# Kernel tuning notes

Measured on AMD Instinct MI355X. Metric: run time of the kernel, lower is better.

The kernel has to match this reference:

```python
import jax, jax.numpy as jnp
import numpy as np

B, S, E, H = 4, 2048, 1024, 16
D = E // H  # head_dim = 64


def setup_inputs() -> dict:
    key = jax.random.key(0)
    ks = jax.random.split(key, 9)
    s = 1.0 / np.sqrt(E)
    return {
        "x": jax.random.normal(ks[0], (B, S, E), dtype=jnp.float32),
        "mask": jnp.ones((B, S), dtype=jnp.int32),
        "Wq": jax.random.uniform(ks[1], (E, E), jnp.float32, -s, s),
        "bq": jnp.zeros((E,), jnp.float32),
        "Wk": jax.random.uniform(ks[2], (E, E), jnp.float32, -s, s),
        "bk": jnp.zeros((E,), jnp.float32),
        "Wv": jax.random.uniform(ks[3], (E, E), jnp.float32, -s, s),
        "bv": jnp.zeros((E,), jnp.float32),
        "Wo": jax.random.uniform(ks[4], (E, E), jnp.float32, -s, s),
        "bo": jnp.zeros((E,), jnp.float32),
    }


def reference(x, mask, Wq, bq, Wk, bk, Wv, bv, Wo, bo):
    # projections: weights stored as (in, out)
    q = x @ Wq + bq  # [B,S,E]
    k = x @ Wk + bk
    v = x @ Wv + bv
    # split heads: b s (h d) -> b h s d
    q = q.reshape(B, S, H, D).transpose(0, 2, 1, 3)
    k = k.reshape(B, S, H, D).transpose(0, 2, 1, 3)
    v = v.reshape(B, S, H, D).transpose(0, 2, 1, 3)
    scale = 1.0 / np.sqrt(D).astype(np.float32)
    dot = jnp.einsum('bhsd,bhtd->bhst', q, k) * scale  # [B,H,S,S]
    # key padding mask: 1 = valid, 0 = masked
    neg_inf = jnp.asarray(-jnp.inf, dot.dtype)
    dot = jnp.where(mask[:, None, None, :] == 0, neg_inf, dot)
    attn = jax.nn.softmax(dot, axis=-1)
    o = jnp.einsum('bhst,bhtd->bhsd', attn, v)  # [B,H,S,D]
    o = o.transpose(0, 2, 1, 3).reshape(B, S, E)  # merge heads
    return o @ Wo + bo
```

## Files before the change

### kernel.cpp

```cpp
#include <hip/hip_runtime.h>

#define Bc 4
#define Sc 2048
#define Ec 1024
#define Hc 16
#define Dc 64
#define BSc 8192
#define KVB 64

typedef short bf16x8 __attribute__((ext_vector_type(8)));
typedef float f32x4 __attribute__((ext_vector_type(4)));
typedef unsigned short u16;
typedef unsigned long long u64;

__device__ __forceinline__ u16 f2bf(float f){
  unsigned u = __builtin_bit_cast(unsigned, f);
  u += 0x7FFFu + ((u >> 16) & 1u);
  return (u16)(u >> 16);
}
__device__ __forceinline__ void gll16(const void* g, void* l){
  __builtin_amdgcn_global_load_lds((const __attribute__((address_space(1))) void*)g,
                                   (__attribute__((address_space(3))) void*)l, 16, 0, 0);
}
__device__ __forceinline__ float exp2_s(float x){
#if __has_builtin(__builtin_amdgcn_exp2f)
  return __builtin_amdgcn_exp2f(x);
#else
  float r;
  asm volatile("v_exp_f32 %0, %1\n\ts_nop 1" : "=v"(r) : "v"(x));
  return r;
#endif
}
__device__ __forceinline__ unsigned cvtpk(float a, float b){
  unsigned r;
  asm volatile("v_cvt_pk_bf16_f32 %0, %1, %2\n\ts_nop 1" : "=v"(r) : "v"(a), "v"(b));
  return r;
}

__global__ void cvt_x_kernel(const float* __restrict__ x, u16* __restrict__ xb, int n){
  int i = (blockIdx.x * 256 + threadIdx.x) * 4;
  if (i >= n) return;
  float4 v = *(const float4*)(x + i);
  *(ushort4*)(xb+i) = make_ushort4(f2bf(v.x), f2bf(v.y), f2bf(v.z), f2bf(v.w));
}

__global__ void wt_kernel(const float* __restrict__ w0, const float* __restrict__ w1,
                          const float* __restrict__ w2, const float* __restrict__ w3,
                          u16* __restrict__ wt){
  const float* w = blockIdx.z==0 ? w0 : blockIdx.z==1 ? w1 : blockIdx.z==2 ? w2 : w3;
  u16* ho = wt + (size_t)blockIdx.z * Ec * Ec;
  __shared__ float t[32][33];
  int k0 = blockIdx.y * 32, n0 = blockIdx.x * 32;
  int tx = threadIdx.x & 31, ty = threadIdx.x >> 5;
  for (int i = 0; i < 4; ++i){
    int k = ty + i*8;
    t[k][tx] = w[(size_t)(k0+k)*Ec + n0 + tx];
  }
  __syncthreads();
  for (int i = 0; i < 4; ++i){
    int nn = ty + i*8;
    ho[(size_t)(n0+nn)*Ec + k0 + tx] = f2bf(t[tx][nn]);
  }
}

__global__ __launch_bounds__(256, 2)
void gemm_qkv(const u16* __restrict__ A, const u16* __restrict__ Wt,
              const float* __restrict__ bq, const float* __restrict__ bk,
              const float* __restrict__ bv,
              u16* __restrict__ qout, u16* __restrict__ kout, u16* __restrict__ vout)
{
  constexpr int K = Ec;
  __shared__ alignas(16) u16 As[128*32];
  __shared__ alignas(16) u16 Bs[128*32];
  const int tid = threadIdx.x, lane = tid & 63, w = tid >> 6;
  const int wr = w >> 1, wc = w & 1;
  const int m0 = blockIdx.y * 128;
  const int n0g = blockIdx.x * 128;
  const int which = n0g >> 10;
  const int n0 = n0g & 1023;
  const u16* Bt = Wt + (size_t)which * Ec * Ec;
  const float* bias = which == 0 ? bq : which == 1 ? bk : bv;
  const int l15 = lane & 15, kslot = lane >> 4;
  const f32x4 fz = {0.f,0.f,0.f,0.f};
  f32x4 acc[4][4];
  for (int i=0;i<4;++i) for (int j=0;j<4;++j) acc[i][j] = fz;

  const int srow = lane >> 2, sslot = lane & 3;

  for (int k0 = 0; k0 < K; k0 += 32){
    __syncthreads();
    for (int i = 0; i < 2; ++i){
      int c = w*2 + i;
      int row = c*16 + srow;
      int sw = (row ^ (row >> 2)) & 3;
      gll16(A  + (size_t)(m0+row)*K + k0 + ((sslot ^ sw) << 3), As + c*512);
      gll16(Bt + (size_t)(n0+row)*K + k0 + ((sslot ^ sw) << 3), Bs + c*512);
    }
    __syncthreads();
    bf16x8 af[4], bfr[4];
    for (int mi = 0; mi < 4; ++mi){
      int row = wr*64 + mi*16 + l15;
      int sw = (row ^ (row >> 2)) & 3;
      af[mi] = *(const bf16x8*)(As + row*32 + ((kslot ^ sw) << 3));
    }
    for (int ni = 0; ni < 4; ++ni){
      int row = wc*64 + ni*16 + l15;
      int sw = (row ^ (row >> 2)) & 3;
      bfr[ni] = *(const bf16x8*)(Bs + row*32 + ((kslot ^ sw) << 3));
    }
    for (int mi = 0; mi < 4; ++mi)
      for (int ni = 0; ni < 4; ++ni)
        acc[mi][ni] = __builtin_amdgcn_mfma_f32_16x16x32_bf16(af[mi], bfr[ni], acc[mi][ni], 0, 0, 0);
  }

  for (int mi = 0; mi < 4; ++mi){
    for (int ni = 0; ni < 4; ++ni){
      int col = n0 + wc*64 + ni*16 + l15;
      int row0 = m0 + wr*64 + mi*16 + kslot*4;
      float bi = bias[col];
      if (which == 2){
        int bb = row0 >> 11, s0 = row0 & 2047;
        int hh = col >> 6, dd = col & 63;
        ushort4 pk = make_ushort4(f2bf(acc[mi][ni][0]+bi), f2bf(acc[mi][ni][1]+bi),
                                  f2bf(acc[mi][ni][2]+bi), f2bf(acc[mi][ni][3]+bi));
        *(ushort4*)(vout + ((size_t)(bb*Hc+hh)*Dc + dd)*Sc + s0) = pk;
      } else {
        u16* dst = which == 0 ? qout : kout;
        for (int j = 0; j < 4; ++j){
          float v = acc[mi][ni][j] + bi;
          int row = row0 + j;
          float vv = (which == 0) ? v * 0.18033688f : v;
          int bb = row >> 11, ss = row & 2047;
          int hh = col >> 6, dd = col & 63;
          dst[((size_t)(bb*Hc+hh)*Sc + ss)*Dc + dd] = f2bf(vv);
        }
      }
    }
  }
}

__global__ __launch_bounds__(256, 2)
void gemm_out(const u16* __restrict__ A, const u16* __restrict__ Bt,
              const float* __restrict__ bias, float* __restrict__ outp)
{
  constexpr int K = Ec;
  __shared__ alignas(16) u16 As[128*32];
  __shared__ alignas(16) u16 Bs[128*32];
  const int tid = threadIdx.x, lane = tid & 63, w = tid >> 6;
  const int wr = w >> 1, wc = w & 1;
  const int m0 = blockIdx.y * 128, n0 = blockIdx.x * 128;
  const int l15 = lane & 15, kslot = lane >> 4;
  const f32x4 fz = {0.f,0.f,0.f,0.f};
  f32x4 acc[4][4];
  for (int i=0;i<4;++i) for (int j=0;j<4;++j) acc[i][j] = fz;

  const int srow = lane >> 2, sslot = lane & 3;

  for (int k0 = 0; k0 < K; k0 += 32){
    __syncthreads();
    for (int i = 0; i < 2; ++i){
      int c = w*2 + i;
      int row = c*16 + srow;
      int sw = (row ^ (row >> 2)) & 3;
      gll16(A  + (size_t)(m0+row)*K + k0 + ((sslot ^ sw) << 3), As + c*512);
      gll16(Bt + (size_t)(n0+row)*K + k0 + ((sslot ^ sw) << 3), Bs + c*512);
    }
    __syncthreads();
    bf16x8 af[4], bfr[4];
    for (int mi = 0; mi < 4; ++mi){
      int row = wr*64 + mi*16 + l15;
      int sw = (row ^ (row >> 2)) & 3;
      af[mi] = *(const bf16x8*)(As + row*32 + ((kslot ^ sw) << 3));
    }
    for (int ni = 0; ni < 4; ++ni){
      int row = wc*64 + ni*16 + l15;
      int sw = (row ^ (row >> 2)) & 3;
      bfr[ni] = *(const bf16x8*)(Bs + row*32 + ((kslot ^ sw) << 3));
    }
    for (int mi = 0; mi < 4; ++mi)
      for (int ni = 0; ni < 4; ++ni)
        acc[mi][ni] = __builtin_amdgcn_mfma_f32_16x16x32_bf16(af[mi], bfr[ni], acc[mi][ni], 0, 0, 0);
  }

  for (int mi = 0; mi < 4; ++mi){
    for (int ni = 0; ni < 4; ++ni){
      int col = n0 + wc*64 + ni*16 + l15;
      int row0 = m0 + wr*64 + mi*16 + kslot*4;
      float bi = bias[col];
      for (int j = 0; j < 4; ++j)
        outp[(size_t)(row0+j)*Ec + col] = acc[mi][ni][j] + bi;
    }
  }
}

__global__ __launch_bounds__(256, 2)
void attn_kernel(const u16* __restrict__ qb, const u16* __restrict__ kb,
                 const u16* __restrict__ vt, const int* __restrict__ mask,
                 u16* __restrict__ ob)
{
  __shared__ alignas(16) u16 Ks[2][KVB*Dc];
  __shared__ alignas(16) u16 Vs[2][Dc*KVB];
  const int tid = threadIdx.x, lane = tid & 63, w = tid >> 6;
  const int l15 = lane & 15, ks = lane >> 4;
  const int wg = ((blockIdx.x & 7) << 7) | (blockIdx.x >> 3);
  const int bh = wg >> 4, qblk = wg & 15;
  const int b = bh >> 4, h = bh & 15;
  const int q0 = qblk*128 + w*32;

  const u16* Q  = qb + (size_t)bh*Sc*Dc;
  const u16* Kg = kb + (size_t)bh*Sc*Dc;
  const u16* Vg = vt + (size_t)bh*Dc*Sc;
  const int* mpb = mask + b*Sc;

  int nzl = 1;
  {
    const int4* mv4 = (const int4*)mpb;
#pragma unroll
    for (int i = 0; i < 8; ++i){
      int4 v = mv4[i*64 + lane];
      nzl &= (v.x && v.y && v.z && v.w) ? 1 : 0;
    }
  }
  const bool allvalid = __all(nzl);

  int koff[2], voff[2];
#pragma unroll
  for (int i = 0; i < 2; ++i){
    int S = (w*2+i)*64 + lane;
    int row = S >> 3, s = S & 7;
    koff[i] = row*Dc + ((s ^ (row & 7)) << 3);
    voff[i] = row*Sc + ((s ^ (row & 7)) << 3);
  }
  const int Xl = (l15 & 7) << 4;

  bf16x8 qf[2][2];
#pragma unroll
  for (int qa = 0; qa < 2; ++qa)
#pragma unroll
    for (int kd = 0; kd < 2; ++kd)
      qf[qa][kd] = *(const bf16x8*)(Q + (size_t)(q0 + qa*16 + l15)*Dc + kd*32 + ks*8);

  bf16x8 onesb;
#pragma unroll
  for (int j = 0; j < 8; ++j) onesb[j] = (short)0x3F80;

  const f32x4 fz = {0.f,0.f,0.f,0.f};
  f32x4 o[2][4];
#pragma unroll
  for (int qa = 0; qa < 2; ++qa)
#pragma unroll
    for (int db = 0; db < 4; ++db) o[qa][db] = fz;
  float m[2] = {-3e38f, -3e38f}, runl[2] = {0.f, 0.f};

#pragma unroll
  for (int i = 0; i < 2; ++i){
    gll16(Kg + koff[i], &Ks[0][(w*2+i)*512]);
    gll16(Vg + voff[i], &Vs[0][(w*2+i)*512]);
  }

  const int NT = Sc / KVB;
  int cur = 0;
  for (int t = 0; t < NT; ++t){
    asm volatile("s_waitcnt vmcnt(0)" ::: "memory");
    __syncthreads();
    if (t + 1 < NT){
      const u16* kg = Kg + (size_t)(t+1)*(KVB*Dc);
      const u16* vg = Vg + (size_t)(t+1)*KVB;
#pragma unroll
      for (int i = 0; i < 2; ++i){
        gll16(kg + koff[i], &Ks[cur^1][(w*2+i)*512]);
        gll16(vg + voff[i], &Vs[cur^1][(w*2+i)*512]);
      }
    }
    const char* Ksb = (const char*)&Ks[cur][0];
    const char* Vsb = (const char*)&Vs[cur][0];

    f32x4 sc[4][2];
#pragma unroll
    for (int nb = 0; nb < 4; ++nb){
      bf16x8 kf0 = *(const bf16x8*)(Ksb + nb*2048 + l15*128 + (((0*4+ks) << 4) ^ Xl));
      bf16x8 kf1 = *(const bf16x8*)(Ksb + nb*2048 + l15*128 + (((1*4+ks) << 4) ^ Xl));
#pragma unroll
      for (int qa = 0; qa < 2; ++qa){
        sc[nb][qa] = __builtin_amdgcn_mfma_f32_16x16x32_bf16(kf0, qf[qa][0], fz, 0,0,0);
        sc[nb][qa] = __builtin_amdgcn_mfma_f32_16x16x32_bf16(kf1, qf[qa][1], sc[nb][qa], 0,0,0);
      }
    }
    if (!allvalid){
      const int* mp = mpb + t*KVB;
#pragma unroll
      for (int nb = 0; nb < 4; ++nb)
#pragma unroll
        for (int r = 0; r < 4; ++r){
          float bi = mp[nb*16 + ks*4 + r] ? 0.f : -3e38f;
          sc[nb][0][r] += bi;
          sc[nb][1][r] += bi;
        }
    }
    float pmax[2];
#pragma unroll
    for (int qa = 0; qa < 2; ++qa){
      f32x4 mx4;
#pragma unroll
      for (int r = 0; r < 4; ++r)
        mx4[r] = fmaxf(fmaxf(sc[0][qa][r], sc[1][qa][r]),
                       fmaxf(sc[2][qa][r], sc[3][qa][r]));
      pmax[qa] = fmaxf(fmaxf(mx4[0], mx4[1]), fmaxf(mx4[2], mx4[3]));
    }
    int ok = (t > 0) && (pmax[0] <= m[0] + 8.f) && (pmax[1] <= m[1] + 8.f);
    if (!__all(ok)){
#pragma unroll
      for (int qa = 0; qa < 2; ++qa){
        float tv = pmax[qa];
        tv = fmaxf(tv, __shfl_xor(tv, 16, 64));
        tv = fmaxf(tv, __shfl_xor(tv, 32, 64));
        float nm = fmaxf(m[qa], tv);
        float al = exp2_s(m[qa] - nm);
        m[qa] = nm;
        runl[qa] *= al;
#pragma unroll
        for (int db = 0; db < 4; ++db)
#pragma unroll
          for (int r = 0; r < 4; ++r)
            o[qa][db][r] *= al;
      }
    }
#pragma unroll
    for (int nb = 0; nb < 4; ++nb)
#pragma unroll
      for (int qa = 0; qa < 2; ++qa)
#pragma unroll
        for (int r = 0; r < 4; ++r)
          sc[nb][qa][r] = exp2_s(sc[nb][qa][r] - m[qa]);

    f32x4 accl[2] = {fz, fz};
#pragma unroll
    for (int kt = 0; kt < 2; ++kt){
      bf16x8 pb[2];
#pragma unroll
      for (int qa = 0; qa < 2; ++qa){
        union { bf16x8 v; unsigned u[4]; } pu;
        pu.u[0] = cvtpk(sc[2*kt  ][qa][0], sc[2*kt  ][qa][1]);
        pu.u[1] = cvtpk(sc[2*kt  ][qa][2], sc[2*kt  ][qa][3]);
        pu.u[2] = cvtpk(sc[2*kt+1][qa][0], sc[2*kt+1][qa][1]);
        pu.u[3] = cvtpk(sc[2*kt+1][qa][2], sc[2*kt+1][qa][3]);
        pb[qa] = pu.v;
      }
      accl[0] = __builtin_amdgcn_mfma_f32_16x16x32_bf16(onesb, pb[0], accl[0], 0,0,0);
      accl[1] = __builtin_amdgcn_mfma_f32_16x16x32_bf16(onesb, pb[1], accl[1], 0,0,0);
#pragma unroll
      for (int db = 0; db < 4; ++db){
        union { bf16x8 v; u64 q[2]; } vu;
        const int g0 = kt*4 + (ks >> 1);
        const int base = db*2048 + l15*128 + (ks & 1)*8;
        vu.q[0] = *(const u64*)(Vsb + base + (((g0    ) << 4) ^ Xl));
        vu.q[1] = *(const u64*)(Vsb + base + (((g0 + 2) << 4) ^ Xl));
#pragma unroll
        for (int qa = 0; qa < 2; ++qa)
          o[qa][db] = __builtin_amdgcn_mfma_f32_16x16x32_bf16(vu.v, pb[qa], o[qa][db], 0,0,0);
      }
    }
    runl[0] += accl[0][0];
    runl[1] += accl[1][0];
    cur ^= 1;
  }
#pragma unroll
  for (int qa = 0; qa < 2; ++qa){
    float inv = __builtin_amdgcn_rcpf(fmaxf(runl[qa], 1e-35f));
    u16* orow = ob + ((size_t)(b*Sc + q0 + qa*16 + l15))*Ec + h*Dc + ks*4;
#pragma unroll
    for (int db = 0; db < 4; ++db){
      ushort4 pk = make_ushort4(f2bf(o[qa][db][0]*inv), f2bf(o[qa][db][1]*inv),
                                f2bf(o[qa][db][2]*inv), f2bf(o[qa][db][3]*inv));
      *(ushort4*)(orow + db*16) = pk;
    }
  }
}

extern "C" void kernel_launch(void* const* d_in, const int* in_sizes, int n_in,
                              void* d_out, int out_size, void* d_ws, size_t ws_size,
                              hipStream_t stream) {
  const float* x  = (const float*)d_in[0];
  const int* mask = (const int*)d_in[1];
  const float* Wq = (const float*)d_in[2];
  const float* bq = (const float*)d_in[3];
  const float* Wk = (const float*)d_in[4];
  const float* bk = (const float*)d_in[5];
  const float* Wv = (const float*)d_in[6];
  const float* bv = (const float*)d_in[7];
  const float* Wo = (const float*)d_in[8];
  const float* bo = (const float*)d_in[9];
  float* out = (float*)d_out;

  u16* ws   = (u16*)d_ws;
  u16* x_bf = ws;
  u16* w_t  = x_bf + (size_t)BSc*Ec;
  u16* q_bf = w_t  + (size_t)4*Ec*Ec;
  u16* k_bf = q_bf + (size_t)BSc*Ec;
  u16* v_t  = k_bf + (size_t)BSc*Ec;
  u16* o_bf = v_t  + (size_t)BSc*Ec;

  cvt_x_kernel<<<BSc*Ec/1024, 256, 0, stream>>>(x, x_bf, BSc*Ec);
  wt_kernel<<<dim3(32,32,4), 256, 0, stream>>>(Wq, Wk, Wv, Wo, w_t);

  const size_t WSZ = (size_t)Ec*Ec;
  gemm_qkv<<<dim3(24,64), 256, 0, stream>>>(x_bf, w_t, bq, bk, bv, q_bf, k_bf, v_t);

  attn_kernel<<<dim3(1024), 256, 0, stream>>>(q_bf, k_bf, v_t, mask, o_bf);

  gemm_out<<<dim3(8,64), 256, 0, stream>>>(o_bf, w_t+3*WSZ, bo, out);
}
```

Measured before the change: 204.3 us.

## Double per-wave query rows in attention to reuse K/V tiles across 64 queries

Each attention wave now handles 64 query rows (four 16-row groups) instead of 32, so a workgroup covers 256 queries and the grid halves to 512 blocks. Every K/V tile loaded into LDS and every fragment read from it feeds twice as many MFMAs, which cuts global and LDS traffic per unit of work. It also swaps the inline-asm v_cvt_pk_bf16 and v_exp fallback for a software bf16 rounding and plain exp2f, which costs more VALU work. The risks are higher register pressure under launch_bounds(256,2) with possible spills, and fewer blocks to spread across the CUs.

```diff
diff --git a/kernel.cpp b/kernel.cpp
--- a/kernel.cpp
+++ b/kernel.cpp
@@ -26,15 +26,8 @@
 #if __has_builtin(__builtin_amdgcn_exp2f)
   return __builtin_amdgcn_exp2f(x);
 #else
-  float r;
-  asm volatile("v_exp_f32 %0, %1\n\ts_nop 1" : "=v"(r) : "v"(x));
-  return r;
+  return exp2f(x);
 #endif
-}
-__device__ __forceinline__ unsigned cvtpk(float a, float b){
-  unsigned r;
-  asm volatile("v_cvt_pk_bf16_f32 %0, %1, %2\n\ts_nop 1" : "=v"(r) : "v"(a), "v"(b));
-  return r;
 }
 
 __global__ void cvt_x_kernel(const float* __restrict__ x, u16* __restrict__ xb, int n){
@@ -202,10 +195,10 @@
   __shared__ alignas(16) u16 Vs[2][Dc*KVB];
   const int tid = threadIdx.x, lane = tid & 63, w = tid >> 6;
   const int l15 = lane & 15, ks = lane >> 4;
-  const int wg = ((blockIdx.x & 7) << 7) | (blockIdx.x >> 3);
-  const int bh = wg >> 4, qblk = wg & 15;
+  const int wg = ((blockIdx.x & 7) << 6) | (blockIdx.x >> 3);
+  const int bh = wg >> 3, qblk = wg & 7;
   const int b = bh >> 4, h = bh & 15;
-  const int q0 = qblk*128 + w*32;
+  const int q0 = qblk*256 + w*64;
 
   const u16* Q  = qb + (size_t)bh*Sc*Dc;
   const u16* Kg = kb + (size_t)bh*Sc*Dc;
@@ -233,9 +226,9 @@
   }
   const int Xl = (l15 & 7) << 4;
 
-  bf16x8 qf[2][2];
-#pragma unroll
-  for (int qa = 0; qa < 2; ++qa)
+  bf16x8 qf[4][2];
+#pragma unroll
+  for (int qa = 0; qa < 4; ++qa)
 #pragma unroll
     for (int kd = 0; kd < 2; ++kd)
       qf[qa][kd] = *(const bf16x8*)(Q + (size_t)(q0 + qa*16 + l15)*Dc + kd*32 + ks*8);
@@ -245,12 +238,12 @@
   for (int j = 0; j < 8; ++j) onesb[j] = (short)0x3F80;
 
   const f32x4 fz = {0.f,0.f,0.f,0.f};
-  f32x4 o[2][4];
-#pragma unroll
-  for (int qa = 0; qa < 2; ++qa)
+  f32x4 o[4][4];
+#pragma unroll
+  for (int qa = 0; qa < 4; ++qa)
 #pragma unroll
     for (int db = 0; db < 4; ++db) o[qa][db] = fz;
-  float m[2] = {-3e38f, -3e38f}, runl[2] = {0.f, 0.f};
+  float m[4] = {-3e38f,-3e38f,-3e38f,-3e38f}, runl[4] = {0.f,0.f,0.f,0.f};
 
 #pragma unroll
   for (int i = 0; i < 2; ++i){
@@ -275,13 +268,13 @@
     const char* Ksb = (const char*)&Ks[cur][0];
     const char* Vsb = (const char*)&Vs[cur][0];
 
-    f32x4 sc[4][2];
+    f32x4 sc[4][4];
 #pragma unroll
     for (int nb = 0; nb < 4; ++nb){
       bf16x8 kf0 = *(const bf16x8*)(Ksb + nb*2048 + l15*128 + (((0*4+ks) << 4) ^ Xl));
       bf16x8 kf1 = *(const bf16x8*)(Ksb + nb*2048 + l15*128 + (((1*4+ks) << 4) ^ Xl));
 #pragma unroll
-      for (int qa = 0; qa < 2; ++qa){
+      for (int qa = 0; qa < 4; ++qa){
         sc[nb][qa] = __builtin_amdgcn_mfma_f32_16x16x32_bf16(kf0, qf[qa][0], fz, 0,0,0);
         sc[nb][qa] = __builtin_amdgcn_mfma_f32_16x16x32_bf16(kf1, qf[qa][1], sc[nb][qa], 0,0,0);
       }
@@ -293,13 +286,13 @@
 #pragma unroll
         for (int r = 0; r < 4; ++r){
           float bi = mp[nb*16 + ks*4 + r] ? 0.f : -3e38f;
-          sc[nb][0][r] += bi;
-          sc[nb][1][r] += bi;
+#pragma unroll
+          for (int qa = 0; qa < 4; ++qa) sc[nb][qa][r] += bi;
         }
     }
-    float pmax[2];
-#pragma unroll
-    for (int qa = 0; qa < 2; ++qa){
+    float pmax[4];
+#pragma unroll
+    for (int qa = 0; qa < 4; ++qa){
       f32x4 mx4;
 #pragma unroll
       for (int r = 0; r < 4; ++r)
@@ -307,10 +300,11 @@
                        fmaxf(sc[2][qa][r], sc[3][qa][r]));
       pmax[qa] = fmaxf(fmaxf(mx4[0], mx4[1]), fmaxf(mx4[2], mx4[3]));
     }
-    int ok = (t > 0) && (pmax[0] <= m[0] + 8.f) && (pmax[1] <= m[1] + 8.f);
+    int ok = (t > 0) && (pmax[0] <= m[0] + 8.f) && (pmax[1] <= m[1] + 8.f)
+                     && (pmax[2] <= m[2] + 8.f) && (pmax[3] <= m[3] + 8.f);
     if (!__all(ok)){
 #pragma unroll
-      for (int qa = 0; qa < 2; ++qa){
+      for (int qa = 0; qa < 4; ++qa){
         float tv = pmax[qa];
         tv = fmaxf(tv, __shfl_xor(tv, 16, 64));
         tv = fmaxf(tv, __shfl_xor(tv, 32, 64));
@@ -328,26 +322,26 @@
 #pragma unroll
     for (int nb = 0; nb < 4; ++nb)
 #pragma unroll
-      for (int qa = 0; qa < 2; ++qa)
+      for (int qa = 0; qa < 4; ++qa)
 #pragma unroll
         for (int r = 0; r < 4; ++r)
           sc[nb][qa][r] = exp2_s(sc[nb][qa][r] - m[qa]);
 
-    f32x4 accl[2] = {fz, fz};
+    f32x4 accl[4] = {fz, fz, fz, fz};
 #pragma unroll
     for (int kt = 0; kt < 2; ++kt){
-      bf16x8 pb[2];
-#pragma unroll
-      for (int qa = 0; qa < 2; ++qa){
-        union { bf16x8 v; unsigned u[4]; } pu;
-        pu.u[0] = cvtpk(sc[2*kt  ][qa][0], sc[2*kt  ][qa][1]);
-        pu.u[1] = cvtpk(sc[2*kt  ][qa][2], sc[2*kt  ][qa][3]);
-        pu.u[2] = cvtpk(sc[2*kt+1][qa][0], sc[2*kt+1][qa][1]);
-        pu.u[3] = cvtpk(sc[2*kt+1][qa][2], sc[2*kt+1][qa][3]);
-        pb[qa] = pu.v;
-      }
-      accl[0] = __builtin_amdgcn_mfma_f32_16x16x32_bf16(onesb, pb[0], accl[0], 0,0,0);
-      accl[1] = __builtin_amdgcn_mfma_f32_16x16x32_bf16(onesb, pb[1], accl[1], 0,0,0);
+      bf16x8 pb[4];
+#pragma unroll
+      for (int qa = 0; qa < 4; ++qa){
+        bf16x8 tb;
+#pragma unroll
+        for (int r = 0; r < 4; ++r){
+          tb[r]     = (short)f2bf(sc[2*kt  ][qa][r]);
+          tb[4 + r] = (short)f2bf(sc[2*kt+1][qa][r]);
+        }
+        pb[qa] = tb;
+        accl[qa] = __builtin_amdgcn_mfma_f32_16x16x32_bf16(onesb, pb[qa], accl[qa], 0,0,0);
+      }
 #pragma unroll
       for (int db = 0; db < 4; ++db){
         union { bf16x8 v; u64 q[2]; } vu;
@@ -356,16 +350,16 @@
         vu.q[0] = *(const u64*)(Vsb + base + (((g0    ) << 4) ^ Xl));
         vu.q[1] = *(const u64*)(Vsb + base + (((g0 + 2) << 4) ^ Xl));
 #pragma unroll
-        for (int qa = 0; qa < 2; ++qa)
+        for (int qa = 0; qa < 4; ++qa)
           o[qa][db] = __builtin_amdgcn_mfma_f32_16x16x32_bf16(vu.v, pb[qa], o[qa][db], 0,0,0);
       }
     }
-    runl[0] += accl[0][0];
-    runl[1] += accl[1][0];
+#pragma unroll
+    for (int qa = 0; qa < 4; ++qa) runl[qa] += accl[qa][0];
     cur ^= 1;
   }
 #pragma unroll
-  for (int qa = 0; qa < 2; ++qa){
+  for (int qa = 0; qa < 4; ++qa){
     float inv = __builtin_amdgcn_rcpf(fmaxf(runl[qa], 1e-35f));
     u16* orow = ob + ((size_t)(b*Sc + q0 + qa*16 + l15))*Ec + h*Dc + ks*4;
 #pragma unroll
@@ -406,7 +400,7 @@
   const size_t WSZ = (size_t)Ec*Ec;
   gemm_qkv<<<dim3(24,64), 256, 0, stream>>>(x_bf, w_t, bq, bk, bv, q_bf, k_bf, v_t);
 
-  attn_kernel<<<dim3(1024), 256, 0, stream>>>(q_bf, k_bf, v_t, mask, o_bf);
+  attn_kernel<<<dim3(512), 256, 0, stream>>>(q_bf, k_bf, v_t, mask, o_bf);
 
   gemm_out<<<dim3(8,64), 256, 0, stream>>>(o_bf, w_t+3*WSZ, bo, out);
 }
```

Result: slower. 216.8 us (+6.1%).
